# Kernel tuning notes

Measured on AMD Instinct MI355X. Metric: run time of the kernel, lower is better.

Reference implementation:

```python
import jax, jax.numpy as jnp
import numpy as np

N = 4096
K = 32
K_NEIGH = 5
LR_EDGE = 0.05
LR_GLOBAL_DECAY = 0.001
NOISE_STD = 0.05
RIPPLE_STRENGTH = 0.01
SPARK_ENERGY_DECAY = 0.98
SPARK_FORCE_STEPS = 5
SPARK_MIN_ENERGY = 0.05
STATE_DECAY = 0.95


def setup_inputs() -> dict:
    key = jax.random.key(0)
    k1, k2, k3 = jax.random.split(key, 3)
    return {
        "W": 0.1 * jax.random.normal(k1, (N, N), jnp.float32),
        "s": jnp.zeros((N,), jnp.float32),
        "noise": jax.random.normal(k2, (N,), jnp.float32),
        "spark_energy": jnp.ones((K,), jnp.float32),
        "u": jax.random.uniform(k3, (K,), jnp.float32),
        "spark_pos": jnp.arange(K, dtype=jnp.int32) % N,
        "spark_age": jnp.zeros((K,), jnp.int32),
    }


def _step(W, s, noise, spark_energy, u, spark_pos, spark_age):
    n = W.shape[0]
    k = spark_pos.shape[0]
    # state diffusion: decay, noisy matvec, sigmoid
    s = s * STATE_DECAY
    s = jax.nn.sigmoid(W @ s + NOISE_STD * noise)
    # force young sparks' positions to 1.0 (drop-mode scatter for masked writes)
    force_idx = jnp.where(spark_age < SPARK_FORCE_STEPS, spark_pos, n)
    s = s.at[force_idx].set(1.0, mode="drop")

    def body(carry, xs):
        W, s = carry
        i, prev, energy, age, ui = xs
        # multinomial over relu(W[prev]) via inverse-CDF on cumsum
        row = W[prev]
        w = jax.nn.relu(row) + 1e-6
        cdf = jnp.cumsum(w)
        nxt = jnp.minimum(
            jnp.searchsorted(cdf, ui * cdf[-1], side="right"), n - 1
        ).astype(prev.dtype)
        # edge learning on traversed edge
        W = W.at[nxt, prev].set(W[nxt, prev] * (1.0 - LR_EDGE) + s[prev] * LR_EDGE)
        # ripple to top-K neighbors of prev (row re-read AFTER edge update, as in torch)
        top = jax.lax.top_k(jax.nn.relu(W[prev]), K_NEIGH)[1]
        W = W.at[prev, top].add(RIPPLE_STRENGTH)
        W = W.at[top, prev].add(RIPPLE_STRENGTH * 0.5)
        W = W.at[top[:, None], top[None, :]].add(RIPPLE_STRENGTH * 0.3)
        # energy decay, deposit energy at new position
        energy = energy * SPARK_ENERGY_DECAY
        s = s.at[nxt].set(energy)
        age = age + 1
        # respawn exhausted sparks
        respawn = energy < SPARK_MIN_ENERGY
        pos_new = jnp.where(respawn, (i % n).astype(prev.dtype), nxt)
        energy = jnp.where(respawn, jnp.float32(1.0), energy)
        age = jnp.where(respawn, jnp.int32(0), age)
        return (W, s), (pos_new, energy, age)

    idx = jnp.arange(k, dtype=jnp.int32)
    (W, s), (pos, energy, age) = jax.lax.scan(
        body, (W, s), (idx, spark_pos, spark_energy, spark_age, u)
    )
    # global decay + clamp
    W = jnp.clip(W * (1.0 - LR_GLOBAL_DECAY), -2.0, 2.0)
    return s, W, pos, energy, age


def reference(W, s, noise, spark_energy, u, spark_pos, spark_age):
    return _step(W, s, noise, spark_energy, u, spark_pos, spark_age)
```

## Files before the change

kernel.cpp:

```cpp
#include <hip/hip_runtime.h>

#define NN 4096
#define KS 32
#define KN 5

typedef float f32x4 __attribute__((ext_vector_type(4)));

#define NB_DEC 512

#define WS_NXT   16384
#define WS_TOPI  16512
#define WS_NEED  (size_t)(WS_TOPI + KS * KN * 4)

__device__ __forceinline__ void merge5(float* av, int* ai,
                                       const float* bv2, const int* bi2) {
    float nv[KN]; int ni[KN];
    int pA = 0, pB = 0;
    #pragma unroll
    for (int q = 0; q < KN; ++q) {
        float va = av[pA];  int ia = ai[pA];
        float vb = bv2[pB]; int ib = bi2[pB];
        bool pickA = (va > vb) || (va == vb && ia < ib);
        if (pickA) { nv[q] = va; ni[q] = ia; ++pA; }
        else       { nv[q] = vb; ni[q] = ib; ++pB; }
    }
    #pragma unroll
    for (int q = 0; q < KN; ++q) { av[q] = nv[q]; ai[q] = ni[q]; }
}

__device__ __forceinline__ void cdf_scan(const float r[4], int tid, int lane, int wid,
                                         double* wave_incl, double incl[4],
                                         double& a_out, double& ascan_out) {
    double a = 0.0;
    #pragma unroll
    for (int m = 0; m < 4; ++m) {
        a += (double)(fmaxf(r[m], 0.f) + 1e-6f);
        incl[m] = a;
    }
    double ascan = a;
    #pragma unroll
    for (int off = 1; off < 64; off <<= 1) {
        double o = __shfl_up(ascan, (unsigned)off, 64);
        if (lane >= off) ascan += o;
    }
    if (lane == 63) wave_incl[wid] = ascan;
    __syncthreads();
    if (tid < 16) {
        double v = wave_incl[tid];
        #pragma unroll
        for (int off = 1; off < 16; off <<= 1) {
            double o = __shfl_up(v, (unsigned)off, 64);
            if (tid >= off) v += o;
        }
        wave_incl[tid] = v;
    }
    __syncthreads();
    a_out = a;
    ascan_out = ascan;
}

__device__ __forceinline__ void block_top5(const float r[4], int tid, int lane, int wid,
                                           float* topv, int* topi, int* dest) {
    float bv[KN]; int bi[KN];
    #pragma unroll
    for (int m = 0; m < 4; ++m) { bv[m] = fmaxf(r[m], 0.f); bi[m] = tid * 4 + m; }
    bv[4] = -1.f; bi[4] = 0x7fffffff;
    #define CE(i, j) { if (bv[i] < bv[j] || (bv[i] == bv[j] && bi[i] > bi[j])) { \
        float tv = bv[i]; bv[i] = bv[j]; bv[j] = tv; \
        int   ti = bi[i]; bi[i] = bi[j]; bi[j] = ti; } }
    CE(0, 1) CE(2, 3) CE(0, 2) CE(1, 3) CE(1, 2)
    #undef CE
    #pragma unroll
    for (int off = 1; off < 64; off <<= 1) {
        float ov[KN]; int oi[KN];
        #pragma unroll
        for (int q = 0; q < KN; ++q) {
            ov[q] = __shfl_xor(bv[q], off, 64);
            oi[q] = __shfl_xor(bi[q], off, 64);
        }
        merge5(bv, bi, ov, oi);
    }
    if (lane == 0) {
        #pragma unroll
        for (int q = 0; q < KN; ++q) { topv[wid * KN + q] = bv[q]; topi[wid * KN + q] = bi[q]; }
    }
    __syncthreads();
    if (tid < 16) {
        #pragma unroll
        for (int q = 0; q < KN; ++q) { bv[q] = topv[tid * KN + q]; bi[q] = topi[tid * KN + q]; }
        #pragma unroll
        for (int off = 1; off < 16; off <<= 1) {
            float ov[KN]; int oi[KN];
            #pragma unroll
            for (int q = 0; q < KN; ++q) {
                ov[q] = __shfl_xor(bv[q], off, 64);
                oi[q] = __shfl_xor(bi[q], off, 64);
            }
            merge5(bv, bi, ov, oi);
        }
        if (tid == 0) {
            #pragma unroll
            for (int q = 0; q < KN; ++q) dest[q] = bi[q];
        }
    }
    __syncthreads();
}

__global__ __launch_bounds__(1024) void k_front(const float* __restrict__ W,
                                                const float* __restrict__ s,
                                                const float* __restrict__ noise,
                                                float* __restrict__ s_out,
                                                float* __restrict__ outW,
                                                const int* __restrict__ pos_in,
                                                const float* __restrict__ u_in,
                                                char* __restrict__ wsb) {
    __shared__ float  sdec[NN];
    __shared__ double wave_incl[16];
    __shared__ float  topv[16 * KN];
    __shared__ int    topi[16 * KN];
    __shared__ int    sh_nxt;
    int tid = threadIdx.x, lane = tid & 63, wid = tid >> 6;
    int bid = blockIdx.x;

    if (bid < NB_DEC) {
        size_t base = (size_t)bid * 8192 + tid;
        const f32x4* Wv = (const f32x4*)W;
        f32x4* Ov = (f32x4*)outW;
        f32x4 v[8];
        #pragma unroll
        for (int r = 0; r < 8; ++r) v[r] = Wv[base + r * 1024];
        #pragma unroll
        for (int r = 0; r < 8; ++r) {
            v[r].x = fminf(fmaxf(v[r].x * 0.999f, -2.f), 2.f);
            v[r].y = fminf(fmaxf(v[r].y * 0.999f, -2.f), 2.f);
            v[r].z = fminf(fmaxf(v[r].z * 0.999f, -2.f), 2.f);
            v[r].w = fminf(fmaxf(v[r].w * 0.999f, -2.f), 2.f);
            __builtin_nontemporal_store(v[r], &Ov[base + r * 1024]);
        }

        if (bid < 256) {
            float4 sv = ((const float4*)s)[tid];
            int nz = (sv.x != 0.f || sv.y != 0.f || sv.z != 0.f || sv.w != 0.f) ? 1 : 0;
            float4 d;
            d.x = sv.x * 0.95f; d.y = sv.y * 0.95f;
            d.z = sv.z * 0.95f; d.w = sv.w * 0.95f;
            ((float4*)sdec)[tid] = d;
            int anynz = __syncthreads_or(nz);
            int row = bid * 16 + wid;
            float acc = 0.f;
            if (anynz) {
                const float4* Wr = (const float4*)(W + (size_t)row * NN);
                for (int it = 0; it < 16; ++it) {
                    float4 w = Wr[it * 64 + lane];
                    int j = (it * 64 + lane) * 4;
                    acc += w.x * sdec[j] + w.y * sdec[j + 1] + w.z * sdec[j + 2] + w.w * sdec[j + 3];
                }
            }
            for (int off = 32; off > 0; off >>= 1) acc += __shfl_down(acc, off, 64);
            if (lane == 0) {
                float y = acc + 0.05f * noise[row];
                s_out[row] = 1.0f / (1.0f + expf(-y));
            }
        }
    } else {
        int kk = bid - NB_DEC;
        int prev = pos_in[kk];
        float4 rv = *((const float4*)(W + (size_t)prev * NN) + tid);
        float r[4] = {rv.x, rv.y, rv.z, rv.w};

        if (tid == 0) sh_nxt = NN - 1;
        double incl[4], a, ascan;
        cdf_scan(r, tid, lane, wid, wave_incl, incl, a, ascan);
        double waveExcl = (wid == 0) ? 0.0 : wave_incl[wid - 1];
        double total    = wave_incl[15];
        double thrIncl  = waveExcl + ascan;
        double thrExcl  = thrIncl - a;
        double t = (double)u_in[kk] * total;
        if (thrIncl > t && thrExcl <= t) {
            int found = 3;
            #pragma unroll
            for (int m = 0; m < 4; ++m)
                if (thrExcl + incl[m] > t) { found = m; break; }
            sh_nxt = tid * 4 + found;
        }
        __syncthreads();
        if (tid == 0) ((int*)(wsb + WS_NXT))[kk] = sh_nxt;

        block_top5(r, tid, lane, wid, topv, topi,
                   (int*)(wsb + WS_TOPI) + kk * KN);
    }
}

__global__ __launch_bounds__(1024) void k_scan(float* __restrict__ W,
                                               const float* __restrict__ s_in,
                                               const float* __restrict__ energy_in,
                                               const float* __restrict__ u_in,
                                               const int* __restrict__ pos_in,
                                               const int* __restrict__ age_in,
                                               float* __restrict__ out,
                                               const char* __restrict__ wsb,
                                               int use_pre) {
    __shared__ float  s_lds[NN];
    __shared__ double wave_incl[16];
    __shared__ float  topv[16 * KN];
    __shared__ int    topi[16 * KN];
    __shared__ int    sh_top[KN];
    __shared__ int    sh_nxt;
    __shared__ unsigned int modlist[KS * 36];
    __shared__ float  preval[KS * 36];
    __shared__ float  res_pos[KS], res_en[KS], res_age[KS];
    __shared__ int    sh_pos[KS], sh_age[KS];
    __shared__ float  sh_u[KS], sh_en[KS];
    __shared__ unsigned char dirty[NN];
    __shared__ int    prenxt_lds[KS];
    __shared__ int    topi_lds[KS * KN];

    int tid = threadIdx.x;
    int lane = tid & 63, wid = tid >> 6;

    ((float4*)s_lds)[tid] = ((const float4*)s_in)[tid];
    ((unsigned int*)dirty)[tid] = 0u;
    if (tid < KS) {
        sh_pos[tid] = pos_in[tid];
        sh_age[tid] = age_in[tid];
        sh_u[tid]   = u_in[tid];
        sh_en[tid]  = energy_in[tid];
    }
    if (use_pre) {
        if (tid < KS)      prenxt_lds[tid] = ((const int*)(wsb + WS_NXT))[tid];
        if (tid < KS * KN) topi_lds[tid]   = ((const int*)(wsb + WS_TOPI))[tid];
    }
    __syncthreads();

    if (use_pre) {
        for (int i = tid; i < KS * 36; i += 1024) {
            int k = i / 36, j = i - k * 36;
            int pv = sh_pos[k], nx = prenxt_lds[k];
            int row, col;
            if (j == 0)       { row = nx;                      col = pv; }
            else if (j < 6)   { row = pv;                      col = topi_lds[k * KN + j - 1]; }
            else if (j < 11)  { row = topi_lds[k * KN + j - 6]; col = pv; }
            else { int q = j - 11; row = topi_lds[k * KN + q / KN]; col = topi_lds[k * KN + q % KN]; }
            unsigned a = (unsigned)(row * NN + col);
            modlist[i] = a;
            preval[i]  = W[a];
        }
    }
    if (tid < KS && sh_age[tid] < 5) s_lds[sh_pos[tid]] = 1.0f;
    __syncthreads();

    for (int k = 0; k < KS; ++k) {
        int prev = sh_pos[k];
        bool rowClean = (use_pre != 0) && (dirty[prev] == 0);
        float r[4] = {0.f, 0.f, 0.f, 0.f};
        bool haveRow = false;
        int nxt;

        if (!rowClean) {
            float4 rv = *((const float4*)(W + (size_t)prev * NN) + tid);
            r[0] = rv.x; r[1] = rv.y; r[2] = rv.z; r[3] = rv.w;
            haveRow = true;
            if (tid == 0) sh_nxt = NN - 1;
            double incl[4], a, ascan;
            cdf_scan(r, tid, lane, wid, wave_incl, incl, a, ascan);
            double waveExcl = (wid == 0) ? 0.0 : wave_incl[wid - 1];
            double total    = wave_incl[15];
            double thrIncl  = waveExcl + ascan;
            double thrExcl  = thrIncl - a;
            double t = (double)sh_u[k] * total;
            if (thrIncl > t && thrExcl <= t) {
                int found = 3;
                #pragma unroll
                for (int m = 0; m < 4; ++m)
                    if (thrExcl + incl[m] > t) { found = m; break; }
                sh_nxt = tid * 4 + found;
            }
            __syncthreads();
            nxt = sh_nxt;
        } else {
            nxt = prenxt_lds[k];
        }

        bool fullTop = !rowClean || (nxt == prev);
        if (fullTop && !haveRow) {
            float4 rv = *((const float4*)(W + (size_t)prev * NN) + tid);
            r[0] = rv.x; r[1] = rv.y; r[2] = rv.z; r[3] = rv.w;
            haveRow = true;
            __syncthreads();
        }

        int t0 = 0, t1 = 0, t2 = 0, t3 = 0, t4 = 0;
        bool usePreval = false, edgeAlias = false;
        if (!fullTop) {
            t0 = topi_lds[k * KN + 0]; t1 = topi_lds[k * KN + 1];
            t2 = topi_lds[k * KN + 2]; t3 = topi_lds[k * KN + 3];
            t4 = topi_lds[k * KN + 4];
            edgeAlias = (nxt == t0) || (nxt == t1) || (nxt == t2) ||
                        (nxt == t3) || (nxt == t4);
            bool aliasP = (prev == t0) || (prev == t1) || (prev == t2) ||
                          (prev == t3) || (prev == t4);
            bool dn = (dirty[nxt] | dirty[t0] | dirty[t1] |
                       dirty[t2]  | dirty[t3] | dirty[t4]) != 0;
            usePreval = !dn && !edgeAlias && !aliasP;
        }

        float sprev = s_lds[prev];
        if (usePreval) {
            if (tid < 36) {
                unsigned a = modlist[k * 36 + tid];
                float v = preval[k * 36 + tid];
                float nv = (tid == 0) ? (v * 0.95f + sprev * 0.05f)
                         : (tid < 6)  ? (v + 0.01f)
                         : (tid < 11) ? (v + 0.005f)
                                      : (v + 0.003f);
                W[a] = nv;
            }
        } else {
            if (tid == 0) {
                size_t o = (size_t)nxt * NN + prev;
                W[o] = W[o] * 0.95f + sprev * 0.05f;
            }
            if (fullTop) {
                if (nxt == prev && tid == (prev >> 2)) {
                    int m = prev & 3;
                    r[m] = r[m] * 0.95f + sprev * 0.05f;
                }
                block_top5(r, tid, lane, wid, topv, topi, sh_top);
                t0 = sh_top[0]; t1 = sh_top[1]; t2 = sh_top[2];
                t3 = sh_top[3]; t4 = sh_top[4];
            } else {
                if (edgeAlias) __syncthreads();
            }
            #define TOPQ(q) (fullTop ? sh_top[q] : topi_lds[k * KN + (q)])
            bool alias = (prev == t0) || (prev == t1) || (prev == t2) ||
                         (prev == t3) || (prev == t4);

            if (alias) {
                if (tid < KN) W[(size_t)prev * NN + TOPQ(tid)] += 0.01f;
                __syncthreads();
                if (tid < KN) W[(size_t)TOPQ(tid) * NN + prev] += 0.005f;
                __syncthreads();
                if (tid < KN * KN) W[(size_t)TOPQ(tid / KN) * NN + TOPQ(tid % KN)] += 0.003f;
            } else {
                if (tid < KN) {
                    W[(size_t)prev * NN + TOPQ(tid)] += 0.01f;
                    W[(size_t)TOPQ(tid) * NN + prev] += 0.005f;
                }
                if (tid >= 64 && tid < 64 + KN * KN) {
                    int q = tid - 64;
                    W[(size_t)TOPQ(q / KN) * NN + TOPQ(q % KN)] += 0.003f;
                }
            }

            if (tid < 36) {
                int row, col;
                if (tid == 0)       { row = nxt;             col = prev; }
                else if (tid < 6)   { row = prev;            col = TOPQ(tid - 1); }
                else if (tid < 11)  { row = TOPQ(tid - 6);   col = prev; }
                else { int q = tid - 11; row = TOPQ(q / KN); col = TOPQ(q % KN); }
                modlist[k * 36 + tid] = (unsigned)(row * NN + col);
            }
            #undef TOPQ
        }

        if (tid == 0) { dirty[nxt] = 1; dirty[prev] = 1; }
        if (tid >= 128 && tid < 128 + KN) {
            int q = tid - 128;
            int tr = fullTop ? sh_top[q] : topi_lds[k * KN + q];
            dirty[tr] = 1;
        }

        if (tid == 0) {
            float en = sh_en[k] * 0.98f;
            s_lds[nxt] = en;
            int age = sh_age[k] + 1;
            int posn = nxt;
            if (en < 0.05f) { posn = k % NN; en = 1.0f; age = 0; }
            res_pos[k] = (float)posn;
            res_en[k]  = en;
            res_age[k] = (float)age;
        }
        __syncthreads();
    }

    ((float4*)out)[tid] = ((float4*)s_lds)[tid];
    if (tid < KS) {
        float* tail = out + NN + (size_t)NN * NN;
        tail[tid]          = res_pos[tid];
        tail[KS + tid]     = res_en[tid];
        tail[2 * KS + tid] = res_age[tid];
    }
    float* outW = out + NN;
    for (int i = tid; i < KS * 36; i += 1024) {
        unsigned idx = modlist[i];
        float v = W[idx] * 0.999f;
        v = fminf(fmaxf(v, -2.f), 2.f);
        outW[idx] = v;
    }
}

extern "C" void kernel_launch(void* const* d_in, const int* in_sizes, int n_in,
                              void* d_out, int out_size, void* d_ws, size_t ws_size,
                              hipStream_t stream) {
    float*       W      = (float*)d_in[0];
    const float* s      = (const float*)d_in[1];
    const float* noise  = (const float*)d_in[2];
    const float* energy = (const float*)d_in[3];
    const float* u      = (const float*)d_in[4];
    const int*   pos    = (const int*)d_in[5];
    const int*   age    = (const int*)d_in[6];
    float*       out    = (float*)d_out;
    float*       s_ws   = (float*)d_ws;

    int use_pre = (ws_size >= WS_NEED) ? 1 : 0;

    k_front<<<NB_DEC + (use_pre ? KS : 0), 1024, 0, stream>>>(
        W, s, noise, s_ws, out + NN, pos, u, (char*)d_ws);
    k_scan<<<1, 1024, 0, stream>>>(W, s_ws, energy, u, pos, age, out,
                                   (const char*)d_ws, use_pre);
}
```

Before: 153.0 us.

## Overlap W decay-copy with serial spark scan, then patch modified entries

Splits the matvec and spark precompute into their own kernel and moves the full W decay/clamp copy into the same launch as the single-block serial scan, so the other 511 blocks stream the copy while block 0 runs the sequential spark loop. Block 0 writes its list of modified indices to workspace, and a small third kernel rewrites those entries after both finish. This hides the serial scan behind the bandwidth-bound copy. The cost is an extra launch, and the scan block now shares memory bandwidth with the copy blocks.

```diff
diff --git a/kernel.cpp b/kernel.cpp
--- a/kernel.cpp
+++ b/kernel.cpp
@@ -6,11 +6,13 @@
 
 typedef float f32x4 __attribute__((ext_vector_type(4)));
 
-#define NB_DEC 512
+#define NB_DEC   512
+#define NB_COMBO 512
 
 #define WS_NXT   16384
 #define WS_TOPI  16512
-#define WS_NEED  (size_t)(WS_TOPI + KS * KN * 4)
+#define WS_MOD   17408
+#define WS_NEED  (size_t)(WS_MOD + KS * 36 * 4)
 
 __device__ __forceinline__ void merge5(float* av, int* ai,
                                        const float* bv2, const int* bi2) {
@@ -106,11 +108,27 @@
     __syncthreads();
 }
 
-__global__ __launch_bounds__(1024) void k_front(const float* __restrict__ W,
+__device__ __forceinline__ void decay_slice(const float* W, float* outW, int d, int tid) {
+    size_t base = (size_t)d * 8192 + tid;
+    const f32x4* Wv = (const f32x4*)W;
+    f32x4* Ov = (f32x4*)outW;
+    f32x4 v[8];
+    #pragma unroll
+    for (int r = 0; r < 8; ++r) v[r] = Wv[base + r * 1024];
+    #pragma unroll
+    for (int r = 0; r < 8; ++r) {
+        v[r].x = fminf(fmaxf(v[r].x * 0.999f, -2.f), 2.f);
+        v[r].y = fminf(fmaxf(v[r].y * 0.999f, -2.f), 2.f);
+        v[r].z = fminf(fmaxf(v[r].z * 0.999f, -2.f), 2.f);
+        v[r].w = fminf(fmaxf(v[r].w * 0.999f, -2.f), 2.f);
+        __builtin_nontemporal_store(v[r], &Ov[base + r * 1024]);
+    }
+}
+
+__global__ __launch_bounds__(1024) void k_mvpre(const float* __restrict__ W,
                                                 const float* __restrict__ s,
                                                 const float* __restrict__ noise,
                                                 float* __restrict__ s_out,
-                                                float* __restrict__ outW,
                                                 const int* __restrict__ pos_in,
                                                 const float* __restrict__ u_in,
                                                 char* __restrict__ wsb) {
@@ -122,48 +140,31 @@
     int tid = threadIdx.x, lane = tid & 63, wid = tid >> 6;
     int bid = blockIdx.x;
 
-    if (bid < NB_DEC) {
-        size_t base = (size_t)bid * 8192 + tid;
-        const f32x4* Wv = (const f32x4*)W;
-        f32x4* Ov = (f32x4*)outW;
-        f32x4 v[8];
-        #pragma unroll
-        for (int r = 0; r < 8; ++r) v[r] = Wv[base + r * 1024];
-        #pragma unroll
-        for (int r = 0; r < 8; ++r) {
-            v[r].x = fminf(fmaxf(v[r].x * 0.999f, -2.f), 2.f);
-            v[r].y = fminf(fmaxf(v[r].y * 0.999f, -2.f), 2.f);
-            v[r].z = fminf(fmaxf(v[r].z * 0.999f, -2.f), 2.f);
-            v[r].w = fminf(fmaxf(v[r].w * 0.999f, -2.f), 2.f);
-            __builtin_nontemporal_store(v[r], &Ov[base + r * 1024]);
-        }
-
-        if (bid < 256) {
-            float4 sv = ((const float4*)s)[tid];
-            int nz = (sv.x != 0.f || sv.y != 0.f || sv.z != 0.f || sv.w != 0.f) ? 1 : 0;
-            float4 d;
-            d.x = sv.x * 0.95f; d.y = sv.y * 0.95f;
-            d.z = sv.z * 0.95f; d.w = sv.w * 0.95f;
-            ((float4*)sdec)[tid] = d;
-            int anynz = __syncthreads_or(nz);
-            int row = bid * 16 + wid;
-            float acc = 0.f;
-            if (anynz) {
-                const float4* Wr = (const float4*)(W + (size_t)row * NN);
-                for (int it = 0; it < 16; ++it) {
-                    float4 w = Wr[it * 64 + lane];
-                    int j = (it * 64 + lane) * 4;
-                    acc += w.x * sdec[j] + w.y * sdec[j + 1] + w.z * sdec[j + 2] + w.w * sdec[j + 3];
-                }
-            }
-            for (int off = 32; off > 0; off >>= 1) acc += __shfl_down(acc, off, 64);
-            if (lane == 0) {
-                float y = acc + 0.05f * noise[row];
-                s_out[row] = 1.0f / (1.0f + expf(-y));
-            }
+    if (bid < 256) {
+        float4 sv = ((const float4*)s)[tid];
+        int nz = (sv.x != 0.f || sv.y != 0.f || sv.z != 0.f || sv.w != 0.f) ? 1 : 0;
+        float4 d;
+        d.x = sv.x * 0.95f; d.y = sv.y * 0.95f;
+        d.z = sv.z * 0.95f; d.w = sv.w * 0.95f;
+        ((float4*)sdec)[tid] = d;
+        int anynz = __syncthreads_or(nz);
+        int row = bid * 16 + wid;
+        float acc = 0.f;
+        if (anynz) {
+            const float4* Wr = (const float4*)(W + (size_t)row * NN);
+            for (int it = 0; it < 16; ++it) {
+                float4 w = Wr[it * 64 + lane];
+                int j = (it * 64 + lane) * 4;
+                acc += w.x * sdec[j] + w.y * sdec[j + 1] + w.z * sdec[j + 2] + w.w * sdec[j + 3];
+            }
+        }
+        for (int off = 32; off > 0; off >>= 1) acc += __shfl_down(acc, off, 64);
+        if (lane == 0) {
+            float y = acc + 0.05f * noise[row];
+            s_out[row] = 1.0f / (1.0f + expf(-y));
         }
     } else {
-        int kk = bid - NB_DEC;
+        int kk = bid - 256;
         int prev = pos_in[kk];
         float4 rv = *((const float4*)(W + (size_t)prev * NN) + tid);
         float r[4] = {rv.x, rv.y, rv.z, rv.w};
@@ -191,15 +192,52 @@
     }
 }
 
-__global__ __launch_bounds__(1024) void k_scan(float* __restrict__ W,
-                                               const float* __restrict__ s_in,
-                                               const float* __restrict__ energy_in,
-                                               const float* __restrict__ u_in,
-                                               const int* __restrict__ pos_in,
-                                               const int* __restrict__ age_in,
-                                               float* __restrict__ out,
-                                               const char* __restrict__ wsb,
-                                               int use_pre) {
+__global__ __launch_bounds__(1024) void k_front(const float* __restrict__ W,
+                                                const float* __restrict__ s,
+                                                const float* __restrict__ noise,
+                                                float* __restrict__ s_out,
+                                                float* __restrict__ outW) {
+    __shared__ float sdec[NN];
+    int tid = threadIdx.x, lane = tid & 63, wid = tid >> 6;
+    int bid = blockIdx.x;
+
+    decay_slice(W, outW, bid, tid);
+
+    if (bid < 256) {
+        float4 sv = ((const float4*)s)[tid];
+        int nz = (sv.x != 0.f || sv.y != 0.f || sv.z != 0.f || sv.w != 0.f) ? 1 : 0;
+        float4 d;
+        d.x = sv.x * 0.95f; d.y = sv.y * 0.95f;
+        d.z = sv.z * 0.95f; d.w = sv.w * 0.95f;
+        ((float4*)sdec)[tid] = d;
+        int anynz = __syncthreads_or(nz);
+        int row = bid * 16 + wid;
+        float acc = 0.f;
+        if (anynz) {
+            const float4* Wr = (const float4*)(W + (size_t)row * NN);
+            for (int it = 0; it < 16; ++it) {
+                float4 w = Wr[it * 64 + lane];
+                int j = (it * 64 + lane) * 4;
+                acc += w.x * sdec[j] + w.y * sdec[j + 1] + w.z * sdec[j + 2] + w.w * sdec[j + 3];
+            }
+        }
+        for (int off = 32; off > 0; off >>= 1) acc += __shfl_down(acc, off, 64);
+        if (lane == 0) {
+            float y = acc + 0.05f * noise[row];
+            s_out[row] = 1.0f / (1.0f + expf(-y));
+        }
+    }
+}
+
+__global__ __launch_bounds__(1024) void k_combo(float* W,
+                                                const float* s_in,
+                                                const float* __restrict__ energy_in,
+                                                const float* __restrict__ u_in,
+                                                const int* __restrict__ pos_in,
+                                                const int* __restrict__ age_in,
+                                                float* out,
+                                                char* wsb,
+                                                int use_pre) {
     __shared__ float  s_lds[NN];
     __shared__ double wave_incl[16];
     __shared__ float  topv[16 * KN];
@@ -217,6 +255,13 @@
 
     int tid = threadIdx.x;
     int lane = tid & 63, wid = tid >> 6;
+    int bid = blockIdx.x;
+
+    if (bid > 0) {
+        decay_slice(W, out + NN, bid - 1, tid);
+        if (bid == NB_COMBO - 1) decay_slice(W, out + NN, NB_COMBO - 1, tid);
+        return;
+    }
 
     ((float4*)s_lds)[tid] = ((const float4*)s_in)[tid];
     ((unsigned int*)dirty)[tid] = 0u;
@@ -390,13 +435,28 @@
         tail[KS + tid]     = res_en[tid];
         tail[2 * KS + tid] = res_age[tid];
     }
-    float* outW = out + NN;
-    for (int i = tid; i < KS * 36; i += 1024) {
-        unsigned idx = modlist[i];
-        float v = W[idx] * 0.999f;
-        v = fminf(fmaxf(v, -2.f), 2.f);
-        outW[idx] = v;
-    }
+    if (gridDim.x == 1) {
+        float* outW = out + NN;
+        for (int i = tid; i < KS * 36; i += 1024) {
+            unsigned idx = modlist[i];
+            float v = W[idx] * 0.999f;
+            v = fminf(fmaxf(v, -2.f), 2.f);
+            outW[idx] = v;
+        }
+    } else {
+        for (int i = tid; i < KS * 36; i += 1024)
+            ((unsigned*)(wsb + WS_MOD))[i] = modlist[i];
+    }
+}
+
+__global__ __launch_bounds__(576) void k_fix(const float* __restrict__ W,
+                                             const char* __restrict__ wsb,
+                                             float* __restrict__ out) {
+    int i = blockIdx.x * 576 + threadIdx.x;
+    unsigned idx = ((const unsigned*)(wsb + WS_MOD))[i];
+    float v = W[idx] * 0.999f;
+    v = fminf(fmaxf(v, -2.f), 2.f);
+    (out + NN)[idx] = v;
 }
 
 extern "C" void kernel_launch(void* const* d_in, const int* in_sizes, int n_in,
@@ -410,12 +470,16 @@
     const int*   pos    = (const int*)d_in[5];
     const int*   age    = (const int*)d_in[6];
     float*       out    = (float*)d_out;
-    float*       s_ws   = (float*)d_ws;
-
-    int use_pre = (ws_size >= WS_NEED) ? 1 : 0;
-
-    k_front<<<NB_DEC + (use_pre ? KS : 0), 1024, 0, stream>>>(
-        W, s, noise, s_ws, out + NN, pos, u, (char*)d_ws);
-    k_scan<<<1, 1024, 0, stream>>>(W, s_ws, energy, u, pos, age, out,
-                                   (const char*)d_ws, use_pre);
-}
+
+    if (ws_size >= WS_NEED) {
+        float* s_ws = (float*)d_ws;
+        k_mvpre<<<256 + KS, 1024, 0, stream>>>(W, s, noise, s_ws, pos, u, (char*)d_ws);
+        k_combo<<<NB_COMBO, 1024, 0, stream>>>(W, s_ws, energy, u, pos, age,
+                                               out, (char*)d_ws, 1);
+        k_fix<<<2, 576, 0, stream>>>(W, (const char*)d_ws, out);
+    } else {
+        k_front<<<NB_DEC, 1024, 0, stream>>>(W, s, noise, out, out + NN);
+        k_combo<<<1, 1024, 0, stream>>>(W, out, energy, u, pos, age,
+                                        out, (char*)d_ws, 0);
+    }
+}
```

Measured after the change: 149.0 us, median of 2. 2.6% less time.
